# Optimization experiments

Measured on AMD Instinct MI355X. Metric: run time of the kernel, lower is better.

The kernel has to match this reference:

```python
import jax, jax.numpy as jnp
import numpy as np

B, S, D = 4, 2048, 1024
INV_SCALE = 32.0  # sqrt(D)


def setup_inputs() -> dict:
    key = jax.random.key(0)
    ks = jax.random.split(key, 7)
    std = 1.0 / np.sqrt(D)
    return {
        "x1": jax.random.normal(ks[0], (B, S, D), dtype=jnp.float32),
        "Wq": jax.random.normal(ks[1], (D, D), dtype=jnp.float32) * std,
        "bq": jax.random.normal(ks[2], (D,), dtype=jnp.float32) * std,
        "Wk": jax.random.normal(ks[3], (D, D), dtype=jnp.float32) * std,
        "bk": jax.random.normal(ks[4], (D,), dtype=jnp.float32) * std,
        "Wv": jax.random.normal(ks[5], (D, D), dtype=jnp.float32) * std,
        "bv": jax.random.normal(ks[6], (D,), dtype=jnp.float32) * std,
    }


def reference(x1, Wq, bq, Wk, bk, Wv, bv):
    # Linear projections (torch Linear: y = x @ W^T + b)
    q = jnp.einsum("bsd,ed->bse", x1, Wq) + bq
    k = jnp.einsum("bsd,ed->bse", x1, Wk) + bk
    v = jnp.einsum("bsd,ed->bse", x1, Wv) + bv
    # Attention: QK^T / inv_scale -> softmax -> (dropout is identity in eval) -> @V
    scores = jnp.einsum("bqd,bkd->bqk", q, k) / INV_SCALE
    attn = jax.nn.softmax(scores, axis=-1)
    out = jnp.einsum("bqk,bkd->bqd", attn, v)
    return out
```

## Files before the change

### kernel.cpp

```cpp
#include <hip/hip_runtime.h>
#include <cstdint>
#include <cstddef>

using bf16 = __bf16;
typedef float f32x4 __attribute__((ext_vector_type(4)));
typedef __bf16 bf16x8v __attribute__((ext_vector_type(8)));
typedef __bf16 bf16x4v __attribute__((ext_vector_type(4)));

#define NX   8388608
#define NW   1048576
#define SB   2048
#define DD   1024

__device__ __forceinline__ void gload_lds16(const bf16* g, bf16* l) {
    __builtin_amdgcn_global_load_lds(
        (const __attribute__((address_space(1))) void*)(g),
        (__attribute__((address_space(3))) void*)(l), 16, 0, 0);
}

__global__ __launch_bounds__(256)
void convert_kernel(const float* __restrict__ x1,
                    const float* __restrict__ Wq, const float* __restrict__ Wk,
                    const float* __restrict__ Wv,
                    const float* __restrict__ bq, const float* __restrict__ bk,
                    const float* __restrict__ bv,
                    bf16* __restrict__ xb, bf16* __restrict__ wb,
                    float* __restrict__ biases)
{
    const int NX4 = NX / 4;
    const int NW4 = NW / 4;
    const int NMAT = NX4 + 3 * NW4;
    const int total = NMAT + 768;
    for (int i = blockIdx.x * 256 + threadIdx.x; i < total; i += gridDim.x * 256) {
        if (i < NMAT) {
            const float* src; bf16* dst; int j;
            if (i < NX4) { src = x1; dst = xb; j = i; }
            else {
                int w = (i - NX4) / NW4;
                j = (i - NX4) - w * NW4;
                src = (w == 0) ? Wq : (w == 1) ? Wk : Wv;
                dst = wb + (size_t)w * NW;
            }
            float4 f = ((const float4*)src)[j];
            bf16x4v o;
            o[0] = (bf16)f.x; o[1] = (bf16)f.y; o[2] = (bf16)f.z; o[3] = (bf16)f.w;
            ((bf16x4v*)dst)[j] = o;
        } else {
            int j = i - NMAT;
            const float* src = (j < 256) ? bq : (j < 512) ? bk : bv;
            ((float4*)biases)[j] = ((const float4*)src)[j & 255];
        }
    }
}

template<int V, typename OutT>
__global__ __launch_bounds__(256)
void gemm_bt(const bf16* __restrict__ A, const bf16* __restrict__ B,
             OutT* __restrict__ C, bf16* __restrict__ vT,
             const float* __restrict__ bias, float* __restrict__ pRow,
             int N, int K, int GRP,
             long sAz, long sBz, long sCz, float scale)
{
    __shared__ bf16 lds[2][2][8192];
    __shared__ float inv[128];
    const int z = blockIdx.z;
    A += (size_t)z * sAz;
    B += (size_t)z * sBz;
    C += (size_t)z * sCz;
    if constexpr (V == 1 || V == 2) pRow += (size_t)z * (SB * 32);

    const int gx = gridDim.x;
    const int gy = gridDim.y;
    const int nwg = gx * gy;
    const int orig = (int)blockIdx.y * gx + (int)blockIdx.x;
    const int q8 = nwg >> 3;
    const int tile = (orig & 7) * q8 + (orig >> 3);
    const int gsz = GRP * gy;
    const int bxg = tile / gsz;
    const int rem = tile - bxg * gsz;
    const int by  = rem / GRP;
    const int bx  = bxg * GRP + (rem - (rem / GRP) * GRP);

    const int n0 = bx * 128;
    const int m0 = by * 128;
    const int t = threadIdx.x;
    const int lane = t & 63;
    const int wid = t >> 6;
    const int wr = wid >> 1, wc = wid & 1;
    const int rl = lane & 15, lg = lane >> 4;

    if constexpr (V == 2) {
        if (t < 128) {
            const float4* pr = (const float4*)&pRow[(size_t)(m0 + t) * 32];
            float s = 0.f;
            #pragma unroll
            for (int j = 0; j < 8; ++j) {
                float4 f = pr[j];
                s += f.x + f.y + f.z + f.w;
            }
            inv[t] = 1.0f / s;
        }
        __syncthreads();
    }

    f32x4 acc[4][4];
    #pragma unroll
    for (int m = 0; m < 4; ++m)
        #pragma unroll
        for (int n = 0; n < 4; ++n) acc[m][n] = (f32x4){0.f, 0.f, 0.f, 0.f};

    auto stage = [&](int b, int k0) {
        #pragma unroll
        for (int l = 0; l < 4; ++l) {
            const int idx = l * 256 + t;
            const int row = idx >> 3;
            const int c   = idx & 7;
            const int gc  = c ^ (row & 7);
            gload_lds16(A + (size_t)(m0 + row) * K + k0 + gc * 8, &lds[b][0][idx * 8]);
            gload_lds16(B + (size_t)(n0 + row) * K + k0 + gc * 8, &lds[b][1][idx * 8]);
        }
    };

    const int NT = K >> 6;

    stage(0, 0);
    stage(1, 64);

    for (int tt = 0; tt < NT; ++tt) {
        const int cur = tt & 1;
        if (tt == NT - 1) asm volatile("s_waitcnt vmcnt(0)" ::: "memory");
        else              asm volatile("s_waitcnt vmcnt(8)" ::: "memory");
        __builtin_amdgcn_s_barrier();

        bf16x8v af[2][4], bfr[2][4];
        #pragma unroll
        for (int kk = 0; kk < 2; ++kk) {
            #pragma unroll
            for (int m = 0; m < 4; ++m) {
                const int row = wr * 64 + m * 16 + rl;
                const int ch  = (kk * 4 + lg) ^ (row & 7);
                af[kk][m] = *(const bf16x8v*)&lds[cur][0][row * 64 + ch * 8];
            }
            #pragma unroll
            for (int n = 0; n < 4; ++n) {
                const int row = wc * 64 + n * 16 + rl;
                const int ch  = (kk * 4 + lg) ^ (row & 7);
                bfr[kk][n] = *(const bf16x8v*)&lds[cur][1][row * 64 + ch * 8];
            }
        }
        asm volatile("s_waitcnt lgkmcnt(0)" ::: "memory");
        __builtin_amdgcn_sched_barrier(0);
        __builtin_amdgcn_s_barrier();

        if (tt + 2 < NT) stage(cur, (tt + 2) * 64);

        #pragma unroll
        for (int kk = 0; kk < 2; ++kk)
            #pragma unroll
            for (int m = 0; m < 4; ++m)
                #pragma unroll
                for (int n = 0; n < 4; ++n)
                    acc[m][n] = __builtin_amdgcn_mfma_f32_16x16x32_bf16(
                        af[kk][m], bfr[kk][n], acc[m][n], 0, 0, 0);
    }

    const int cif = rl;
    const int rif = lg << 2;

    if constexpr (V == 1) {
        const float sc2 = scale * 1.4426950408889634f;
        const float sh2 = -8.656170245333781f;
        float rs[4][4];
        #pragma unroll
        for (int m = 0; m < 4; ++m)
            #pragma unroll
            for (int r = 0; r < 4; ++r) rs[m][r] = 0.f;

        #pragma unroll
        for (int m = 0; m < 4; ++m) {
            const int gm = m0 + wr * 64 + m * 16 + rif;
            #pragma unroll
            for (int n = 0; n < 4; ++n) {
                const int col = n0 + wc * 64 + n * 16 + cif;
                #pragma unroll
                for (int r = 0; r < 4; ++r) {
                    const float e = exp2f(fmaf(acc[m][n][r], sc2, sh2));
                    rs[m][r] += e;
                    C[(size_t)(gm + r) * N + col] = (OutT)e;
                }
            }
        }
        #pragma unroll
        for (int m = 0; m < 4; ++m)
            #pragma unroll
            for (int r = 0; r < 4; ++r) {
                #pragma unroll
                for (int msk = 1; msk < 16; msk <<= 1)
                    rs[m][r] += __shfl_xor(rs[m][r], msk);
            }
        if ((lane & 15) == 0) {
            const int slot = bx * 2 + wc;
            #pragma unroll
            for (int m = 0; m < 4; ++m) {
                const int gm = m0 + wr * 64 + m * 16 + rif;
                #pragma unroll
                for (int r = 0; r < 4; ++r)
                    pRow[(size_t)(gm + r) * 32 + slot] = rs[m][r];
            }
        }
    } else if constexpr (V == 0) {
        if (n0 >= 2048) {
            bf16* T = &lds[0][0][0];
            __syncthreads();
            #pragma unroll
            for (int m = 0; m < 4; ++m) {
                const int sl = wr * 64 + m * 16 + rif;
                #pragma unroll
                for (int n = 0; n < 4; ++n) {
                    const int dl = wc * 64 + n * 16 + cif;
                    const float bb = bias[n0 + dl];
                    bf16x4v pk;
                    #pragma unroll
                    for (int r = 0; r < 4; ++r) pk[r] = (bf16)(acc[m][n][r] + bb);
                    *(bf16x4v*)&T[dl * 132 + sl] = pk;
                }
            }
            __syncthreads();
            const int d  = t >> 1;
            const int sh = (t & 1) << 6;
            const int batch = m0 >> 11;
            const int dg = n0 - 2048 + d;
            const int sg = (m0 & 2047) + sh;
            uint4* dst = (uint4*)&vT[((size_t)batch << 21) + ((size_t)dg << 11) + sg];
            const uint2* srcp = (const uint2*)&T[d * 132 + sh];
            #pragma unroll
            for (int j = 0; j < 8; ++j) {
                uint2 a = srcp[2 * j], b2 = srcp[2 * j + 1];
                dst[j] = (uint4){a.x, a.y, b2.x, b2.y};
            }
        } else {
            #pragma unroll
            for (int m = 0; m < 4; ++m) {
                const int gm = m0 + wr * 64 + m * 16 + rif;
                #pragma unroll
                for (int n = 0; n < 4; ++n) {
                    const int col = n0 + wc * 64 + n * 16 + cif;
                    const float bb = bias[col];
                    if (col < 1024) {
                        #pragma unroll
                        for (int r = 0; r < 4; ++r)
                            C[(size_t)(gm + r) * 1024 + col] = (OutT)(acc[m][n][r] + bb);
                    } else {
                        #pragma unroll
                        for (int r = 0; r < 4; ++r)
                            C[NX + (size_t)(gm + r) * 1024 + (col - 1024)] = (OutT)(acc[m][n][r] + bb);
                    }
                }
            }
        }
    } else {
        #pragma unroll
        for (int m = 0; m < 4; ++m) {
            const int gm = m0 + wr * 64 + m * 16 + rif;
            const int rloc = wr * 64 + m * 16 + rif;
            #pragma unroll
            for (int n = 0; n < 4; ++n) {
                const int col = n0 + wc * 64 + n * 16 + cif;
                #pragma unroll
                for (int r = 0; r < 4; ++r)
                    C[(size_t)(gm + r) * N + col] = (OutT)(acc[m][n][r] * inv[rloc + r]);
            }
        }
    }
}

extern "C" void kernel_launch(void* const* d_in, const int* in_sizes, int n_in,
                              void* d_out, int out_size, void* d_ws, size_t ws_size,
                              hipStream_t stream)
{
    const float* x1 = (const float*)d_in[0];
    const float* Wq = (const float*)d_in[1];
    const float* bq = (const float*)d_in[2];
    const float* Wk = (const float*)d_in[3];
    const float* bk = (const float*)d_in[4];
    const float* Wv = (const float*)d_in[5];
    const float* bv = (const float*)d_in[6];
    float* out = (float*)d_out;

    bf16* xb     = (bf16*)d_ws;
    bf16* wb     = xb + NX;
    bf16* qkb    = wb + 3 * NW;
    bf16* vTb    = qkb + 2 * (size_t)NX;
    bf16* scores = vTb + NX;
    float* biases = (float*)(scores + 4 * (size_t)SB * SB);
    float* partial = (float*)xb;

    convert_kernel<<<dim3(2048), dim3(256), 0, stream>>>(
        x1, Wq, Wk, Wv, bq, bk, bv, xb, wb, biases);

    gemm_bt<0, bf16><<<dim3(24, 64, 1), dim3(256), 0, stream>>>(
        xb, wb, qkb, vTb, biases, nullptr, 1024, 1024, 8, 0L, 0L, 0L, 1.0f);

    gemm_bt<1, bf16><<<dim3(16, 16, 4), dim3(256), 0, stream>>>(
        qkb, qkb + NX, scores, nullptr, nullptr, partial, SB, DD, 16,
        (long)(SB * DD), (long)(SB * DD), (long)(SB * SB), 1.0f / 32.0f);

    gemm_bt<2, float><<<dim3(8, 16, 4), dim3(256), 0, stream>>>(
        scores, vTb, out, nullptr, nullptr, partial, DD, SB, 8,
        (long)(SB * SB), (long)(SB * DD), (long)(SB * DD), 1.0f);
}
```

Measured before the change: 156.3 us.

## Replace QKV projection GEMM with persistent kernel looping over Q/K/V phases

The QKV projection is moved out of the generic templated GEMM into a dedicated kernel. It launches 512 workgroups, and each one computes the same row tile for the Q, K and V column blocks in three sequential phases, so the A tile stays warm in cache across phases. Q/K outputs are now staged through LDS and written as coalesced 16-byte rows instead of scattered scalar stores. The trade-off is fewer concurrent workgroups and extra LDS round-trips and barriers per phase.

```diff
diff --git a/kernel.cpp b/kernel.cpp
--- a/kernel.cpp
+++ b/kernel.cpp
@@ -53,6 +53,146 @@
     }
 }
 
+__global__ __launch_bounds__(256)
+void qkv_persist(const bf16* __restrict__ A, const bf16* __restrict__ B,
+                 bf16* __restrict__ C, bf16* __restrict__ vT,
+                 const float* __restrict__ bias)
+{
+    __shared__ bf16 lds[2][2][8192];
+    const int K = 1024;
+    const int b0 = blockIdx.y >> 3;
+    const int by = ((blockIdx.y & 7) << 3) | blockIdx.x;
+    const int m0 = by * 128;
+
+    const int t = threadIdx.x;
+    const int lane = t & 63;
+    const int wid = t >> 6;
+    const int wr = wid >> 1, wc = wid & 1;
+    const int rl = lane & 15, lg = lane >> 4;
+
+    bf16* T = &lds[0][0][0];
+
+    for (int ph = 0; ph < 3; ++ph) {
+        const int n0 = (ph * 8 + b0) * 128;
+
+        f32x4 acc[4][4];
+        #pragma unroll
+        for (int m = 0; m < 4; ++m)
+            #pragma unroll
+            for (int n = 0; n < 4; ++n) acc[m][n] = (f32x4){0.f, 0.f, 0.f, 0.f};
+
+        auto stage = [&](int b, int k0) {
+            #pragma unroll
+            for (int l = 0; l < 4; ++l) {
+                const int idx = l * 256 + t;
+                const int row = idx >> 3;
+                const int c   = idx & 7;
+                const int gc  = c ^ (row & 7);
+                gload_lds16(A + (size_t)(m0 + row) * K + k0 + gc * 8, &lds[b][0][idx * 8]);
+                gload_lds16(B + (size_t)(n0 + row) * K + k0 + gc * 8, &lds[b][1][idx * 8]);
+            }
+        };
+
+        stage(0, 0);
+        stage(1, 64);
+
+        for (int tt = 0; tt < 16; ++tt) {
+            const int cur = tt & 1;
+            if (tt == 15) asm volatile("s_waitcnt vmcnt(0)" ::: "memory");
+            else          asm volatile("s_waitcnt vmcnt(8)" ::: "memory");
+            __builtin_amdgcn_s_barrier();
+
+            bf16x8v af[2][4], bfr[2][4];
+            #pragma unroll
+            for (int kk = 0; kk < 2; ++kk) {
+                #pragma unroll
+                for (int m = 0; m < 4; ++m) {
+                    const int row = wr * 64 + m * 16 + rl;
+                    const int ch  = (kk * 4 + lg) ^ (row & 7);
+                    af[kk][m] = *(const bf16x8v*)&lds[cur][0][row * 64 + ch * 8];
+                }
+                #pragma unroll
+                for (int n = 0; n < 4; ++n) {
+                    const int row = wc * 64 + n * 16 + rl;
+                    const int ch  = (kk * 4 + lg) ^ (row & 7);
+                    bfr[kk][n] = *(const bf16x8v*)&lds[cur][1][row * 64 + ch * 8];
+                }
+            }
+            asm volatile("s_waitcnt lgkmcnt(0)" ::: "memory");
+            __builtin_amdgcn_sched_barrier(0);
+            __builtin_amdgcn_s_barrier();
+
+            if (tt + 2 < 16) stage(cur, (tt + 2) * 64);
+
+            #pragma unroll
+            for (int kk = 0; kk < 2; ++kk)
+                #pragma unroll
+                for (int m = 0; m < 4; ++m)
+                    #pragma unroll
+                    for (int n = 0; n < 4; ++n)
+                        acc[m][n] = __builtin_amdgcn_mfma_f32_16x16x32_bf16(
+                            af[kk][m], bfr[kk][n], acc[m][n], 0, 0, 0);
+        }
+
+        const int cif = rl;
+        const int rif = lg << 2;
+
+        if (ph < 2) {
+            #pragma unroll
+            for (int m = 0; m < 4; ++m) {
+                const int sl = wr * 64 + m * 16 + rif;
+                #pragma unroll
+                for (int n = 0; n < 4; ++n) {
+                    const int dl = wc * 64 + n * 16 + cif;
+                    const float bbv = bias[n0 + dl];
+                    #pragma unroll
+                    for (int r = 0; r < 4; ++r)
+                        T[(sl + r) * 132 + dl] = (bf16)(acc[m][n][r] + bbv);
+                }
+            }
+            __syncthreads();
+            const int s  = t >> 1;
+            const int hh = (t & 1) << 6;
+            bf16* dst = (ph == 0 ? C : C + NX)
+                        + (size_t)(m0 + s) * 1024 + (n0 & 1023) + hh;
+            const uint2* srcp = (const uint2*)&T[s * 132 + hh];
+            #pragma unroll
+            for (int j = 0; j < 8; ++j) {
+                uint2 a = srcp[2 * j], b2 = srcp[2 * j + 1];
+                ((uint4*)dst)[j] = (uint4){a.x, a.y, b2.x, b2.y};
+            }
+        } else {
+            #pragma unroll
+            for (int m = 0; m < 4; ++m) {
+                const int sl = wr * 64 + m * 16 + rif;
+                #pragma unroll
+                for (int n = 0; n < 4; ++n) {
+                    const int dl = wc * 64 + n * 16 + cif;
+                    const float bbv = bias[n0 + dl];
+                    bf16x4v pk;
+                    #pragma unroll
+                    for (int r = 0; r < 4; ++r) pk[r] = (bf16)(acc[m][n][r] + bbv);
+                    *(bf16x4v*)&T[dl * 132 + sl] = pk;
+                }
+            }
+            __syncthreads();
+            const int d  = t >> 1;
+            const int sh = (t & 1) << 6;
+            const int batch = m0 >> 11;
+            const int dg = n0 - 2048 + d;
+            const int sg = (m0 & 2047) + sh;
+            uint4* dst = (uint4*)&vT[((size_t)batch << 21) + ((size_t)dg << 11) + sg];
+            const uint2* srcp = (const uint2*)&T[d * 132 + sh];
+            #pragma unroll
+            for (int j = 0; j < 8; ++j) {
+                uint2 a = srcp[2 * j], b2 = srcp[2 * j + 1];
+                dst[j] = (uint4){a.x, a.y, b2.x, b2.y};
+            }
+        }
+        __syncthreads();
+    }
+}
+
 template<int V, typename OutT>
 __global__ __launch_bounds__(256)
 void gemm_bt(const bf16* __restrict__ A, const bf16* __restrict__ B,
@@ -67,7 +207,7 @@
     A += (size_t)z * sAz;
     B += (size_t)z * sBz;
     C += (size_t)z * sCz;
-    if constexpr (V == 1 || V == 2) pRow += (size_t)z * (SB * 32);
+    pRow += (size_t)z * (SB * 32);
 
     const int gx = gridDim.x;
     const int gy = gridDim.y;
@@ -206,56 +346,6 @@
                 #pragma unroll
                 for (int r = 0; r < 4; ++r)
                     pRow[(size_t)(gm + r) * 32 + slot] = rs[m][r];
-            }
-        }
-    } else if constexpr (V == 0) {
-        if (n0 >= 2048) {
-            bf16* T = &lds[0][0][0];
-            __syncthreads();
-            #pragma unroll
-            for (int m = 0; m < 4; ++m) {
-                const int sl = wr * 64 + m * 16 + rif;
-                #pragma unroll
-                for (int n = 0; n < 4; ++n) {
-                    const int dl = wc * 64 + n * 16 + cif;
-                    const float bb = bias[n0 + dl];
-                    bf16x4v pk;
-                    #pragma unroll
-                    for (int r = 0; r < 4; ++r) pk[r] = (bf16)(acc[m][n][r] + bb);
-                    *(bf16x4v*)&T[dl * 132 + sl] = pk;
-                }
-            }
-            __syncthreads();
-            const int d  = t >> 1;
-            const int sh = (t & 1) << 6;
-            const int batch = m0 >> 11;
-            const int dg = n0 - 2048 + d;
-            const int sg = (m0 & 2047) + sh;
-            uint4* dst = (uint4*)&vT[((size_t)batch << 21) + ((size_t)dg << 11) + sg];
-            const uint2* srcp = (const uint2*)&T[d * 132 + sh];
-            #pragma unroll
-            for (int j = 0; j < 8; ++j) {
-                uint2 a = srcp[2 * j], b2 = srcp[2 * j + 1];
-                dst[j] = (uint4){a.x, a.y, b2.x, b2.y};
-            }
-        } else {
-            #pragma unroll
-            for (int m = 0; m < 4; ++m) {
-                const int gm = m0 + wr * 64 + m * 16 + rif;
-                #pragma unroll
-                for (int n = 0; n < 4; ++n) {
-                    const int col = n0 + wc * 64 + n * 16 + cif;
-                    const float bb = bias[col];
-                    if (col < 1024) {
-                        #pragma unroll
-                        for (int r = 0; r < 4; ++r)
-                            C[(size_t)(gm + r) * 1024 + col] = (OutT)(acc[m][n][r] + bb);
-                    } else {
-                        #pragma unroll
-                        for (int r = 0; r < 4; ++r)
-                            C[NX + (size_t)(gm + r) * 1024 + (col - 1024)] = (OutT)(acc[m][n][r] + bb);
-                    }
-                }
             }
         }
     } else {
@@ -298,8 +388,8 @@
     convert_kernel<<<dim3(2048), dim3(256), 0, stream>>>(
         x1, Wq, Wk, Wv, bq, bk, bv, xb, wb, biases);
 
-    gemm_bt<0, bf16><<<dim3(24, 64, 1), dim3(256), 0, stream>>>(
-        xb, wb, qkb, vTb, biases, nullptr, 1024, 1024, 8, 0L, 0L, 0L, 1.0f);
+    qkv_persist<<<dim3(8, 64), dim3(256), 0, stream>>>(
+        xb, wb, qkb, vTb, biases);
 
     gemm_bt<1, bf16><<<dim3(16, 16, 4), dim3(256), 0, stream>>>(
         qkb, qkb + NX, scores, nullptr, nullptr, partial, SB, DD, 16,
```

After: 183.2 us. 1.17x slower.
